# Kernel optimization log

Measured on AMD Instinct MI355X. Metric: run time of the kernel, lower is better.

Reference implementation:

```python
import jax, jax.numpy as jnp
import numpy as np

B, M, A, F = 8, 512, 16, 128  # batch, atoms/messages, irrep dim (n_ang_mom**2=16), feature channels
CG_DENSITY = 0.25             # CG coefficient tensors are highly sparse; emulate with a random mask


def setup_inputs() -> dict:
    key = jax.random.key(0)
    kx, ky, kc, km = jax.random.split(key, 4)
    x = jax.random.normal(kx, (B, M, A, F), dtype=jnp.float32)
    y = jax.random.normal(ky, (B, M, A, F), dtype=jnp.float32)
    # stand-in for cgc_multiplier(n_ang_mom): sparse [a, d, c] Clebsch-Gordan coefficient tensor
    cgc_dense = jax.random.normal(kc, (A, A, A), dtype=jnp.float32)
    mask = jax.random.bernoulli(km, CG_DENSITY, (A, A, A))
    cgc = jnp.where(mask, cgc_dense, 0.0)
    return {"x": x, "y": y, "cgc": cgc}


def reference(x, y, cgc):
    # TensorProductContractionLayer.call: triple contraction over irrep indices a, c
    # x: [b,m,a,f], y: [b,m,c,f], cgc: [a,d,c] -> res: [b,m,d,f]
    return jnp.einsum('bmaf,bmcf,adc->bmdf', x, y, cgc)
```

## Files before the change

kernel.cpp:

```cpp
#include <hip/hip_runtime.h>
#include <hip/hip_bf16.h>


typedef __attribute__((ext_vector_type(8))) short  short8;
typedef __attribute__((ext_vector_type(4))) float  floatx4;
typedef __attribute__((ext_vector_type(4))) unsigned int uintx4;

#define AA 16
#define FF 128

static __device__ __forceinline__ unsigned int pack_bf16_2(float lo, float hi) {
    __hip_bfloat162 h = __float22bfloat162_rn(make_float2(lo, hi));
    unsigned int u;
    __builtin_memcpy(&u, &h, 4);
    return u;
}

static __device__ __forceinline__ void gload_lds16(const float* g, float* l) {
    __builtin_amdgcn_global_load_lds(
        (const __attribute__((address_space(1))) void*)g,
        (__attribute__((address_space(3))) void*)l,
        16, 0, 0);
}

__global__ __launch_bounds__(256, 4)
void tpc_mfma_lds_kernel(const float* __restrict__ x,
                         const float* __restrict__ y,
                         const float* __restrict__ cgc,
                         float* __restrict__ out) {
    __shared__ float lx[AA * FF];
    __shared__ float ly[AA * FF];

    const int tid  = threadIdx.x;
    const int w    = tid >> 6;
    const int lane = tid & 63;
    const int L    = lane & 15;
    const int quad = lane >> 4;
    const int qh   = quad >> 1;
    const int c0   = (quad & 1) * 8;

    const int bm = blockIdx.x;
    const float* xb = x   + (size_t)bm * (AA * FF);
    const float* yb = y   + (size_t)bm * (AA * FF);
    float*       ob = out + (size_t)bm * (AA * FF);

    {
        const int off = w * 512 + lane * 4;
        gload_lds16(xb + off,       lx + off);
        gload_lds16(xb + off + 256, lx + off + 256);
        gload_lds16(yb + off,       ly + off);
        gload_lds16(yb + off + 256, ly + off + 256);
    }

    short8 wfrag[8];
#pragma unroll
    for (int t = 0; t < 8; ++t) {
        const float* wp = cgc + (2 * t + qh) * (AA * AA) + L * AA + c0;
        const floatx4 w0 = *(const floatx4*)(wp);
        const floatx4 w1 = *(const floatx4*)(wp + 4);
        uintx4 u;
        u.x = pack_bf16_2(w0.x, w0.y);
        u.y = pack_bf16_2(w0.z, w0.w);
        u.z = pack_bf16_2(w1.x, w1.y);
        u.w = pack_bf16_2(w1.z, w1.w);
        wfrag[t] = __builtin_bit_cast(short8, u);
    }

    __syncthreads();

    const int f0 = w * 32 + L;

    float xvA[8], xvB[8], yvA[8], yvB[8];
#pragma unroll
    for (int j = 0; j < 8; ++j) {
        yvA[j] = ly[(c0 + j) * FF + f0];
        yvB[j] = ly[(c0 + j) * FF + f0 + 16];
    }
#pragma unroll
    for (int t = 0; t < 8; ++t) {
        xvA[t] = lx[(2 * t + qh) * FF + f0];
        xvB[t] = lx[(2 * t + qh) * FF + f0 + 16];
    }

    floatx4 acc0 = {0.f, 0.f, 0.f, 0.f};
    floatx4 acc1 = {0.f, 0.f, 0.f, 0.f};
#pragma unroll
    for (int t = 0; t < 8; ++t) {
        uintx4 u;
        float xs = xvA[t];
        u.x = pack_bf16_2(xs * yvA[0], xs * yvA[1]);
        u.y = pack_bf16_2(xs * yvA[2], xs * yvA[3]);
        u.z = pack_bf16_2(xs * yvA[4], xs * yvA[5]);
        u.w = pack_bf16_2(xs * yvA[6], xs * yvA[7]);
        acc0 = __builtin_amdgcn_mfma_f32_16x16x32_bf16(
                   wfrag[t], __builtin_bit_cast(short8, u), acc0, 0, 0, 0);

        xs = xvB[t];
        u.x = pack_bf16_2(xs * yvB[0], xs * yvB[1]);
        u.y = pack_bf16_2(xs * yvB[2], xs * yvB[3]);
        u.z = pack_bf16_2(xs * yvB[4], xs * yvB[5]);
        u.w = pack_bf16_2(xs * yvB[6], xs * yvB[7]);
        acc1 = __builtin_amdgcn_mfma_f32_16x16x32_bf16(
                   wfrag[t], __builtin_bit_cast(short8, u), acc1, 0, 0, 0);
    }

#pragma unroll
    for (int r = 0; r < 4; ++r) {
        const int row = (quad * 4 + r) * FF;
        ob[row + f0]      = acc0[r];
        ob[row + f0 + 16] = acc1[r];
    }
}

extern "C" void kernel_launch(void* const* d_in, const int* in_sizes, int n_in,
                              void* d_out, int out_size, void* d_ws, size_t ws_size,
                              hipStream_t stream) {
    const float* x   = (const float*)d_in[0];
    const float* y   = (const float*)d_in[1];
    const float* cgc = (const float*)d_in[2];
    float* out = (float*)d_out;

    hipLaunchKernelGGL(tpc_mfma_lds_kernel, dim3(4096), dim3(256), 0, stream,
                       x, y, cgc, out);
}
```

Measured before the change: 107.9 us.

## Process four batch-rows per block with double-buffered LDS prefetch

Each block now handles four consecutive (b,m) slices instead of one, and the grid shrinks to a quarter of its size. While one slice is being computed, the async global-to-LDS loads for the next slice are issued into a second shared buffer, with one barrier per iteration. This is meant to overlap memory latency with compute and to amortise the per-block setup, including the conversion of the CG weight fragments. In exchange it doubles LDS use per block and leaves fewer blocks resident for hiding latency. The compiler may also insert conservative waits that limit the overlap.

Measured after the change: 107.1 us. No clear change (-0.7%).

```diff
diff --git a/kernel.cpp b/kernel.cpp
--- a/kernel.cpp
+++ b/kernel.cpp
@@ -8,6 +8,7 @@
 
 #define AA 16
 #define FF 128
+#define BM_PER_BLOCK 4
 
 static __device__ __forceinline__ unsigned int pack_bf16_2(float lo, float hi) {
     __hip_bfloat162 h = __float22bfloat162_rn(make_float2(lo, hi));
@@ -24,12 +25,12 @@
 }
 
 __global__ __launch_bounds__(256, 4)
-void tpc_mfma_lds_kernel(const float* __restrict__ x,
-                         const float* __restrict__ y,
-                         const float* __restrict__ cgc,
-                         float* __restrict__ out) {
-    __shared__ float lx[AA * FF];
-    __shared__ float ly[AA * FF];
+void tpc_mfma_pipe_kernel(const float* __restrict__ x,
+                          const float* __restrict__ y,
+                          const float* __restrict__ cgc,
+                          float* __restrict__ out) {
+    __shared__ float lx[2][AA * FF];
+    __shared__ float ly[2][AA * FF];
 
     const int tid  = threadIdx.x;
     const int w    = tid >> 6;
@@ -39,17 +40,17 @@
     const int qh   = quad >> 1;
     const int c0   = (quad & 1) * 8;
 
-    const int bm = blockIdx.x;
-    const float* xb = x   + (size_t)bm * (AA * FF);
-    const float* yb = y   + (size_t)bm * (AA * FF);
-    float*       ob = out + (size_t)bm * (AA * FF);
+    const int bm0 = blockIdx.x * BM_PER_BLOCK;
+    const size_t stride = (size_t)(AA * FF);
+    const int off = w * 512 + lane * 4;
 
     {
-        const int off = w * 512 + lane * 4;
-        gload_lds16(xb + off,       lx + off);
-        gload_lds16(xb + off + 256, lx + off + 256);
-        gload_lds16(yb + off,       ly + off);
-        gload_lds16(yb + off + 256, ly + off + 256);
+        const float* xb = x + (size_t)bm0 * stride;
+        const float* yb = y + (size_t)bm0 * stride;
+        gload_lds16(xb + off,       &lx[0][off]);
+        gload_lds16(xb + off + 256, &lx[0][off + 256]);
+        gload_lds16(yb + off,       &ly[0][off]);
+        gload_lds16(yb + off + 256, &ly[0][off + 256]);
     }
 
     short8 wfrag[8];
@@ -70,45 +71,66 @@
 
     const int f0 = w * 32 + L;
 
-    float xvA[8], xvB[8], yvA[8], yvB[8];
 #pragma unroll
-    for (int j = 0; j < 8; ++j) {
-        yvA[j] = ly[(c0 + j) * FF + f0];
-        yvB[j] = ly[(c0 + j) * FF + f0 + 16];
-    }
+    for (int i = 0; i < BM_PER_BLOCK; ++i) {
+        const int cur = i & 1;
+
+        if (i + 1 < BM_PER_BLOCK) {
+            const int nxt = (i + 1) & 1;
+            const float* xb = x + (size_t)(bm0 + i + 1) * stride;
+            const float* yb = y + (size_t)(bm0 + i + 1) * stride;
+            gload_lds16(xb + off,       &lx[nxt][off]);
+            gload_lds16(xb + off + 256, &lx[nxt][off + 256]);
+            gload_lds16(yb + off,       &ly[nxt][off]);
+            gload_lds16(yb + off + 256, &ly[nxt][off + 256]);
+        }
+
+        const float* lxc = lx[cur];
+        const float* lyc = ly[cur];
+
+        float xvA[8], xvB[8], yvA[8], yvB[8];
 #pragma unroll
-    for (int t = 0; t < 8; ++t) {
-        xvA[t] = lx[(2 * t + qh) * FF + f0];
-        xvB[t] = lx[(2 * t + qh) * FF + f0 + 16];
-    }
+        for (int j = 0; j < 8; ++j) {
+            yvA[j] = lyc[(c0 + j) * FF + f0];
+            yvB[j] = lyc[(c0 + j) * FF + f0 + 16];
+        }
+#pragma unroll
+        for (int t = 0; t < 8; ++t) {
+            xvA[t] = lxc[(2 * t + qh) * FF + f0];
+            xvB[t] = lxc[(2 * t + qh) * FF + f0 + 16];
+        }
 
-    floatx4 acc0 = {0.f, 0.f, 0.f, 0.f};
-    floatx4 acc1 = {0.f, 0.f, 0.f, 0.f};
+        floatx4 acc0 = {0.f, 0.f, 0.f, 0.f};
+        floatx4 acc1 = {0.f, 0.f, 0.f, 0.f};
 #pragma unroll
-    for (int t = 0; t < 8; ++t) {
-        uintx4 u;
-        float xs = xvA[t];
-        u.x = pack_bf16_2(xs * yvA[0], xs * yvA[1]);
-        u.y = pack_bf16_2(xs * yvA[2], xs * yvA[3]);
-        u.z = pack_bf16_2(xs * yvA[4], xs * yvA[5]);
-        u.w = pack_bf16_2(xs * yvA[6], xs * yvA[7]);
-        acc0 = __builtin_amdgcn_mfma_f32_16x16x32_bf16(
-                   wfrag[t], __builtin_bit_cast(short8, u), acc0, 0, 0, 0);
+        for (int t = 0; t < 8; ++t) {
+            uintx4 u;
+            float xs = xvA[t];
+            u.x = pack_bf16_2(xs * yvA[0], xs * yvA[1]);
+            u.y = pack_bf16_2(xs * yvA[2], xs * yvA[3]);
+            u.z = pack_bf16_2(xs * yvA[4], xs * yvA[5]);
+            u.w = pack_bf16_2(xs * yvA[6], xs * yvA[7]);
+            acc0 = __builtin_amdgcn_mfma_f32_16x16x32_bf16(
+                       wfrag[t], __builtin_bit_cast(short8, u), acc0, 0, 0, 0);
 
-        xs = xvB[t];
-        u.x = pack_bf16_2(xs * yvB[0], xs * yvB[1]);
-        u.y = pack_bf16_2(xs * yvB[2], xs * yvB[3]);
-        u.z = pack_bf16_2(xs * yvB[4], xs * yvB[5]);
-        u.w = pack_bf16_2(xs * yvB[6], xs * yvB[7]);
-        acc1 = __builtin_amdgcn_mfma_f32_16x16x32_bf16(
-                   wfrag[t], __builtin_bit_cast(short8, u), acc1, 0, 0, 0);
-    }
+            xs = xvB[t];
+            u.x = pack_bf16_2(xs * yvB[0], xs * yvB[1]);
+            u.y = pack_bf16_2(xs * yvB[2], xs * yvB[3]);
+            u.z = pack_bf16_2(xs * yvB[4], xs * yvB[5]);
+            u.w = pack_bf16_2(xs * yvB[6], xs * yvB[7]);
+            acc1 = __builtin_amdgcn_mfma_f32_16x16x32_bf16(
+                       wfrag[t], __builtin_bit_cast(short8, u), acc1, 0, 0, 0);
+        }
 
+        float* ob = out + (size_t)(bm0 + i) * stride;
 #pragma unroll
-    for (int r = 0; r < 4; ++r) {
-        const int row = (quad * 4 + r) * FF;
-        ob[row + f0]      = acc0[r];
-        ob[row + f0 + 16] = acc1[r];
+        for (int r = 0; r < 4; ++r) {
+            const int row = (quad * 4 + r) * FF;
+            ob[row + f0]      = acc0[r];
+            ob[row + f0 + 16] = acc1[r];
+        }
+
+        __syncthreads();
     }
 }
 
@@ -120,6 +142,6 @@
     const float* cgc = (const float*)d_in[2];
     float* out = (float*)d_out;
 
-    hipLaunchKernelGGL(tpc_mfma_lds_kernel, dim3(4096), dim3(256), 0, stream,
+    hipLaunchKernelGGL(tpc_mfma_pipe_kernel, dim3(1024), dim3(256), 0, stream,
                        x, y, cgc, out);
 }
```

## Double-buffer per-wave LDS staging over four rows and drop block barrier

Applied to the files above, without the earlier changes.

Each block now handles four (b,m) rows instead of one, launching a quarter as many blocks. Each wave stages only its own 32-feature column slice of x and y into a private double-buffered LDS region, which removes the need for __syncthreads. While one row is being computed, the next row is prefetched, with manual s_waitcnt vmcnt counts controlling the pipeline. This aims to hide global-load latency and amortise the cgc fragment setup across rows. In exchange it relies on hand-tuned vmcnt values that assume stores also count toward vmcnt, and it gives the scheduler fewer blocks to spread across the GPU.

Measured after the change: 108.4 us. No clear change (+0.5%).

```diff
diff --git a/kernel.cpp b/kernel.cpp
--- a/kernel.cpp
+++ b/kernel.cpp
@@ -8,6 +8,7 @@
 
 #define AA 16
 #define FF 128
+#define NBM 4
 
 static __device__ __forceinline__ unsigned int pack_bf16_2(float lo, float hi) {
     __hip_bfloat162 h = __float22bfloat162_rn(make_float2(lo, hi));
@@ -24,12 +25,11 @@
 }
 
 __global__ __launch_bounds__(256, 4)
-void tpc_mfma_lds_kernel(const float* __restrict__ x,
-                         const float* __restrict__ y,
-                         const float* __restrict__ cgc,
-                         float* __restrict__ out) {
-    __shared__ float lx[AA * FF];
-    __shared__ float ly[AA * FF];
+void tpc_mfma_nobar_kernel(const float* __restrict__ x,
+                           const float* __restrict__ y,
+                           const float* __restrict__ cgc,
+                           float* __restrict__ out) {
+    __shared__ float lds[4 * 2 * 1024];
 
     const int tid  = threadIdx.x;
     const int w    = tid >> 6;
@@ -39,18 +39,25 @@
     const int qh   = quad >> 1;
     const int c0   = (quad & 1) * 8;
 
-    const int bm = blockIdx.x;
-    const float* xb = x   + (size_t)bm * (AA * FF);
-    const float* yb = y   + (size_t)bm * (AA * FF);
-    float*       ob = out + (size_t)bm * (AA * FF);
+    const int bm0 = blockIdx.x * NBM;
+    const size_t stride = (size_t)(AA * FF);
 
-    {
-        const int off = w * 512 + lane * 4;
-        gload_lds16(xb + off,       lx + off);
-        gload_lds16(xb + off + 256, lx + off + 256);
-        gload_lds16(yb + off,       ly + off);
-        gload_lds16(yb + off + 256, ly + off + 256);
+    float* wl = lds + w * 2048;
+    const int g_l   = (lane >> 3) * FF + w * 32 + (lane & 7) * 4;
+    const int l_l   = lane * 4;
+
+#define STAGE(bmi, buf)                                                        \
+    {                                                                          \
+        const float* xb_ = x + (size_t)(bmi) * stride;                         \
+        const float* yb_ = y + (size_t)(bmi) * stride;                         \
+        float* lb_ = wl + (buf) * 1024;                                        \
+        gload_lds16(xb_ + g_l,          lb_ + l_l);                            \
+        gload_lds16(xb_ + 8 * FF + g_l, lb_ + 256 + l_l);                      \
+        gload_lds16(yb_ + g_l,          lb_ + 512 + l_l);                      \
+        gload_lds16(yb_ + 8 * FF + g_l, lb_ + 768 + l_l);                      \
     }
+
+    STAGE(bm0, 0);
 
     short8 wfrag[8];
 #pragma unroll
@@ -66,50 +73,65 @@
         wfrag[t] = __builtin_bit_cast(short8, u);
     }
 
-    __syncthreads();
-
-    const int f0 = w * 32 + L;
-
-    float xvA[8], xvB[8], yvA[8], yvB[8];
-#pragma unroll
-    for (int j = 0; j < 8; ++j) {
-        yvA[j] = ly[(c0 + j) * FF + f0];
-        yvB[j] = ly[(c0 + j) * FF + f0 + 16];
-    }
-#pragma unroll
-    for (int t = 0; t < 8; ++t) {
-        xvA[t] = lx[(2 * t + qh) * FF + f0];
-        xvB[t] = lx[(2 * t + qh) * FF + f0 + 16];
-    }
-
-    floatx4 acc0 = {0.f, 0.f, 0.f, 0.f};
-    floatx4 acc1 = {0.f, 0.f, 0.f, 0.f};
-#pragma unroll
-    for (int t = 0; t < 8; ++t) {
-        uintx4 u;
-        float xs = xvA[t];
-        u.x = pack_bf16_2(xs * yvA[0], xs * yvA[1]);
-        u.y = pack_bf16_2(xs * yvA[2], xs * yvA[3]);
-        u.z = pack_bf16_2(xs * yvA[4], xs * yvA[5]);
-        u.w = pack_bf16_2(xs * yvA[6], xs * yvA[7]);
-        acc0 = __builtin_amdgcn_mfma_f32_16x16x32_bf16(
-                   wfrag[t], __builtin_bit_cast(short8, u), acc0, 0, 0, 0);
-
-        xs = xvB[t];
-        u.x = pack_bf16_2(xs * yvB[0], xs * yvB[1]);
-        u.y = pack_bf16_2(xs * yvB[2], xs * yvB[3]);
-        u.z = pack_bf16_2(xs * yvB[4], xs * yvB[5]);
-        u.w = pack_bf16_2(xs * yvB[6], xs * yvB[7]);
-        acc1 = __builtin_amdgcn_mfma_f32_16x16x32_bf16(
-                   wfrag[t], __builtin_bit_cast(short8, u), acc1, 0, 0, 0);
-    }
+    STAGE(bm0 + 1, 1);
 
 #pragma unroll
-    for (int r = 0; r < 4; ++r) {
-        const int row = (quad * 4 + r) * FF;
-        ob[row + f0]      = acc0[r];
-        ob[row + f0 + 16] = acc1[r];
+    for (int i = 0; i < NBM; ++i) {
+        if (i + 1 < NBM) {
+            asm volatile("s_waitcnt vmcnt(12)" ::: "memory");
+        } else {
+            asm volatile("s_waitcnt vmcnt(8)" ::: "memory");
+        }
+
+        const float* lb = wl + (i & 1) * 1024;
+
+        float xvA[8], xvB[8], yvA[8], yvB[8];
+#pragma unroll
+        for (int j = 0; j < 8; ++j) {
+            yvA[j] = lb[512 + (c0 + j) * 32 + L];
+            yvB[j] = lb[512 + (c0 + j) * 32 + L + 16];
+        }
+#pragma unroll
+        for (int t = 0; t < 8; ++t) {
+            xvA[t] = lb[(2 * t + qh) * 32 + L];
+            xvB[t] = lb[(2 * t + qh) * 32 + L + 16];
+        }
+
+        floatx4 acc0 = {0.f, 0.f, 0.f, 0.f};
+        floatx4 acc1 = {0.f, 0.f, 0.f, 0.f};
+#pragma unroll
+        for (int t = 0; t < 8; ++t) {
+            uintx4 u;
+            float xs = xvA[t];
+            u.x = pack_bf16_2(xs * yvA[0], xs * yvA[1]);
+            u.y = pack_bf16_2(xs * yvA[2], xs * yvA[3]);
+            u.z = pack_bf16_2(xs * yvA[4], xs * yvA[5]);
+            u.w = pack_bf16_2(xs * yvA[6], xs * yvA[7]);
+            acc0 = __builtin_amdgcn_mfma_f32_16x16x32_bf16(
+                       wfrag[t], __builtin_bit_cast(short8, u), acc0, 0, 0, 0);
+
+            xs = xvB[t];
+            u.x = pack_bf16_2(xs * yvB[0], xs * yvB[1]);
+            u.y = pack_bf16_2(xs * yvB[2], xs * yvB[3]);
+            u.z = pack_bf16_2(xs * yvB[4], xs * yvB[5]);
+            u.w = pack_bf16_2(xs * yvB[6], xs * yvB[7]);
+            acc1 = __builtin_amdgcn_mfma_f32_16x16x32_bf16(
+                       wfrag[t], __builtin_bit_cast(short8, u), acc1, 0, 0, 0);
+        }
+
+        float* ob = out + (size_t)(bm0 + i) * stride;
+        const int fg = w * 32 + L;
+#pragma unroll
+        for (int r = 0; r < 4; ++r) {
+            const int row = (quad * 4 + r) * FF;
+            ob[row + fg]      = acc0[r];
+            ob[row + fg + 16] = acc1[r];
+        }
+
+        if (i + 2 < NBM)
+            STAGE(bm0 + i + 2, i & 1);
     }
+#undef STAGE
 }
 
 extern "C" void kernel_launch(void* const* d_in, const int* in_sizes, int n_in,
@@ -120,6 +142,6 @@
     const float* cgc = (const float*)d_in[2];
     float* out = (float*)d_out;
 
-    hipLaunchKernelGGL(tpc_mfma_lds_kernel, dim3(4096), dim3(256), 0, stream,
+    hipLaunchKernelGGL(tpc_mfma_nobar_kernel, dim3(1024), dim3(256), 0, stream,
                        x, y, cgc, out);
 }
```
